# Optimization experiments

Hardware: AMD Instinct MI355X
Metric: run time of the kernel (lower is better)

## Reference

```python
import jax, jax.numpy as jnp
import numpy as np

P, B, L = 32, 64, 128
E, HB, HP = 64, 128, 128   # byte emb dim, byte GRU hidden, packet GRU hidden
PE = 2 * HB                # packet embedding dim = 256
LH = 128                   # attention linear hidden
NC = 10                    # num classes


def _gru_dir(x, w_ih, w_hh, b_ih, b_hh, reverse=False):
    # x: [T, N, E_in] -> outputs [T, N, H]; PyTorch GRU gate math, h0 = 0.
    H = w_hh.shape[1]
    xg = jnp.einsum('tne,ge->tng', x, w_ih) + b_ih  # precompute input gates [T,N,3H]
    if reverse:
        xg = xg[::-1]

    def step(h, xgt):
        hg = h @ w_hh.T + b_hh
        xr, xz, xn = jnp.split(xgt, 3, axis=-1)
        hr, hz, hn = jnp.split(hg, 3, axis=-1)
        r = jax.nn.sigmoid(xr + hr)
        z = jax.nn.sigmoid(xz + hz)
        n = jnp.tanh(xn + r * hn)
        h = (1.0 - z) * n + z * h
        return h, h

    h0 = jnp.zeros((x.shape[1], H), x.dtype)
    _, ys = jax.lax.scan(step, h0, xg)
    if reverse:
        ys = ys[::-1]
    return ys


def _bigru(x, wif, whf, bif, bhf, wib, whb, bib, bhb):
    f = _gru_dir(x, wif, whf, bif, bhf, reverse=False)
    b = _gru_dir(x, wib, whb, bib, bhb, reverse=True)
    return jnp.concatenate([f, b], axis=-1)


def setup_inputs() -> dict:
    key = jax.random.key(0)
    ks = jax.random.split(key, 32)
    rn = lambda k, shp: (jax.random.normal(k, shp, dtype=jnp.float32) * 0.05)
    inp = {}
    inp['flow'] = jax.random.randint(ks[0], (P, B, L), 0, 256, dtype=jnp.int64)
    inp['emb'] = rn(ks[1], (256, E))
    # byte biGRU (forward / backward dirs)
    inp['byte_wih_f'] = rn(ks[2], (3 * HB, E)); inp['byte_whh_f'] = rn(ks[3], (3 * HB, HB))
    inp['byte_bih_f'] = rn(ks[4], (3 * HB,));   inp['byte_bhh_f'] = rn(ks[5], (3 * HB,))
    inp['byte_wih_b'] = rn(ks[6], (3 * HB, E)); inp['byte_whh_b'] = rn(ks[7], (3 * HB, HB))
    inp['byte_bih_b'] = rn(ks[8], (3 * HB,));   inp['byte_bhh_b'] = rn(ks[9], (3 * HB,))
    # packet biGRU
    inp['pkt_wih_f'] = rn(ks[10], (3 * HP, PE)); inp['pkt_whh_f'] = rn(ks[11], (3 * HP, HP))
    inp['pkt_bih_f'] = rn(ks[12], (3 * HP,));    inp['pkt_bhh_f'] = rn(ks[13], (3 * HP,))
    inp['pkt_wih_b'] = rn(ks[14], (3 * HP, PE)); inp['pkt_whh_b'] = rn(ks[15], (3 * HP, HP))
    inp['pkt_bih_b'] = rn(ks[16], (3 * HP,));    inp['pkt_bhh_b'] = rn(ks[17], (3 * HP,))
    # byte attention (Linear(2HB->LH), Linear(LH->1))
    inp['ba_w1'] = rn(ks[18], (LH, 2 * HB)); inp['ba_b1'] = rn(ks[19], (LH,))
    inp['ba_w2'] = rn(ks[20], (1, LH));      inp['ba_b2'] = rn(ks[21], (1,))
    # packet attention (Linear(2HP->LH), Linear(LH->1))
    inp['pa_w1'] = rn(ks[22], (LH, 2 * HP)); inp['pa_b1'] = rn(ks[23], (LH,))
    inp['pa_w2'] = rn(ks[24], (1, LH));      inp['pa_b2'] = rn(ks[25], (1,))
    # final classifier
    inp['wf'] = rn(ks[26], (NC, 2 * HP)); inp['bf'] = rn(ks[27], (NC,))
    return inp


def reference(flow, emb,
              byte_wih_f, byte_whh_f, byte_bih_f, byte_bhh_f,
              byte_wih_b, byte_whh_b, byte_bih_b, byte_bhh_b,
              pkt_wih_f, pkt_whh_f, pkt_bih_f, pkt_bhh_f,
              pkt_wih_b, pkt_whh_b, pkt_bih_b, pkt_bhh_b,
              ba_w1, ba_b1, ba_w2, ba_b2,
              pa_w1, pa_b1, pa_w2, pa_b2,
              wf, bf):
    p, b, l = flow.shape
    x = emb[flow]                                   # [P,B,L,E]
    # batch the per-packet byte GRU across packets: [L, P*B, E]
    xb = x.transpose(2, 0, 1, 3).reshape(l, p * b, E)
    out = _bigru(xb, byte_wih_f, byte_whh_f, byte_bih_f, byte_bhh_f,
                 byte_wih_b, byte_whh_b, byte_bih_b, byte_bhh_b)  # [L, P*B, 2HB]
    out = out.reshape(l, p, b, 2 * HB)
    # Attention: tanh(lin1) -> lin2 -> softmax over dim=1 of the [L,B,1] view,
    # i.e. over the batch axis (faithful to the original code).
    h = jnp.tanh(jnp.einsum('lpbd,hd->lpbh', out, ba_w1) + ba_b1)
    score = jnp.einsum('lpbh,oh->lpbo', h, ba_w2) + ba_b2          # [L,P,B,1]
    attn = jax.nn.softmax(score, axis=2)
    packet_emb = (out * attn).sum(axis=0)                          # [P,B,2HB]
    # packet biGRU over packet sequence
    out2 = _bigru(packet_emb, pkt_wih_f, pkt_whh_f, pkt_bih_f, pkt_bhh_f,
                  pkt_wih_b, pkt_whh_b, pkt_bih_b, pkt_bhh_b)      # [P,B,2HP]
    h2 = jnp.tanh(jnp.einsum('pbd,hd->pbh', out2, pa_w1) + pa_b1)
    score2 = jnp.einsum('pbh,oh->pbo', h2, pa_w2) + pa_b2          # [P,B,1]
    attn2 = jax.nn.softmax(score2, axis=1)
    flow_emb = (out2 * attn2).sum(axis=1)                          # [P,2HP] (faithful sum over dim=1)
    return flow_emb @ wf.T + bf                                    # [P,NC]
```

## Files before the change

kernel.cpp:

```cpp
#include <hip/hip_runtime.h>
#include <hip/hip_bf16.h>
#include <hip/hip_fp16.h>
#include <cstdint>
#include <cstddef>


#define DINLINE __device__ __forceinline__

typedef _Float16 f16;
typedef f16 f16x8 __attribute__((ext_vector_type(8)));
typedef float f32x4 __attribute__((ext_vector_type(4)));

#define SCL_RZ (-1.44269504089f)
#define SCL_N (2.88539008178f)

static DINLINE float fast_tanh(float x) {
    const float e = __builtin_amdgcn_exp2f(2.88539008178f * x);
    return 1.0f - 2.0f * __builtin_amdgcn_rcpf(1.0f + e);
}

static DINLINE void lds_barrier() {
    asm volatile("s_waitcnt lgkmcnt(0)\n\ts_barrier" ::: "memory");
    __builtin_amdgcn_sched_barrier(0);
}

__global__ void k_tables_w1(const float* __restrict__ emb,
                            const float* __restrict__ wihF, const float* __restrict__ bihF,
                            const float* __restrict__ bhhF,
                            const float* __restrict__ wihB, const float* __restrict__ bihB,
                            const float* __restrict__ bhhB,
                            float4* __restrict__ tab4F, float4* __restrict__ tab4B,
                            const float* __restrict__ w1, f16* __restrict__ w1h) {
    if (blockIdx.x >= 512) {
        const int col = blockIdx.x - 512;
        const int k = threadIdx.x;
        if (k < 256)
            w1h[col * 256 + (k ^ ((col & 7) << 3))] =
                (f16)(SCL_N * w1[col * 256 + k]);
        return;
    }
    const int v = blockIdx.x & 255;
    const int dir = blockIdx.x >> 8;
    const float* wih = dir ? wihB : wihF;
    const float* bih = dir ? bihB : bihF;
    const float* bhh = dir ? bhhB : bhhF;
    float4* tab4 = dir ? tab4B : tab4F;
    __shared__ float er[64];
    __shared__ float sh[384];
    if (threadIdx.x < 64) er[threadIdx.x] = emb[v * 64 + threadIdx.x];
    __syncthreads();
    const int g = threadIdx.x;
    float acc = bih[g] + (g < 256 ? bhh[g] : 0.0f);
    #pragma unroll
    for (int e = 0; e < 64; ++e) acc = fmaf(wih[g * 64 + e], er[e], acc);
    sh[g] = acc * (g < 256 ? SCL_RZ : SCL_N);
    __syncthreads();
    if (g < 128) {
        float4 pk;
        pk.x = sh[g];
        pk.y = sh[g + 128];
        pk.z = sh[g + 256];
        pk.w = 0.f;
        tab4[v * 128 + g] = pk;
    }
}

struct TransArgs {
    const float* src[2];
    float* dst[2];
    int R[2];
    int C[2];
};
__global__ void k_transpose(TransArgs a) {
    const int m = blockIdx.y;
    const float* __restrict__ s = a.src[m];
    float* __restrict__ d = a.dst[m];
    const int R = a.R[m], C = a.C[m];
    const int total = R * C;
    for (int idx = blockIdx.x * blockDim.x + threadIdx.x; idx < total;
         idx += gridDim.x * blockDim.x) {
        const int r = idx / C, c = idx - r * C;
        d[c * R + r] = s[idx];
    }
}

__global__ __launch_bounds__(512, 1) void k_byte_gru(
    const int* __restrict__ flow,
    const float4* __restrict__ tab4F, const float4* __restrict__ tab4B,
    const float* __restrict__ whhF, const float* __restrict__ whhB,
    const float* __restrict__ bhhF, const float* __restrict__ bhhB,
    __half* __restrict__ hF, __half* __restrict__ hB) {
    const int dir = blockIdx.x & 1;
    const int chunk = blockIdx.x >> 1;
    const int row0 = chunk * 16;
    const int tid = threadIdx.x;
    const int wid = tid >> 6;
    const int lane = tid & 63;
    const int c = lane & 15;
    const int q = lane >> 4;
    const int j = wid * 16 + c;

    const float4* __restrict__ t4 = dir ? tab4B : tab4F;
    const float* __restrict__ whh = dir ? whhB : whhF;
    const float* __restrict__ bhh = dir ? bhhB : bhhF;
    __half* __restrict__ hout = dir ? hB : hF;

    __shared__ f16 hbuf[2][16 * 128];
    __shared__ int flow_lds[16][128];

    for (int i = tid; i < 16 * 128; i += 512)
        flow_lds[i >> 7][i & 127] = flow[row0 * 128 + i] & 255;
    for (int i = tid; i < 16 * 128; i += 512) hbuf[0][i] = (f16)0.f;

    f16x8 Bf[3][4];
    #pragma unroll
    for (int g = 0; g < 3; ++g) {
        const float scl = (g == 2) ? SCL_N : SCL_RZ;
        #pragma unroll
        for (int ks = 0; ks < 4; ++ks) {
            const float* src = whh + (size_t)(g * 128 + j) * 128 + ks * 32 + q * 8;
            f16x8 b;
            #pragma unroll
            for (int e = 0; e < 8; ++e) b[e] = (f16)(scl * src[e]);
            Bf[g][ks] = b;
        }
    }
    const float bh2 = SCL_N * bhh[j + 256];
    float hold[4];
    #pragma unroll
    for (int rr = 0; rr < 4; ++rr) hold[rr] = 0.f;
    __syncthreads();

    for (int t = 0; t < 128; ++t) {
        const int curb = t & 1, nxtb = curb ^ 1;
        const int tt = dir ? (127 - t) : t;

        float4 x4[4];
        #pragma unroll
        for (int rr = 0; rr < 4; ++rr)
            x4[rr] = t4[flow_lds[q * 4 + rr][tt] * 128 + j];

        f16x8 Af[4];
        #pragma unroll
        for (int ks = 0; ks < 4; ++ks) {
            const int kb = ks * 32 + q * 8;
            const int idx = c * 128 + (kb ^ ((c & 7) << 3));
            Af[ks] = *reinterpret_cast<const f16x8*>(&hbuf[curb][idx]);
        }

        f32x4 a0 = {0.f, 0.f, 0.f, 0.f};
        f32x4 a1 = {0.f, 0.f, 0.f, 0.f};
        f32x4 a2 = {0.f, 0.f, 0.f, 0.f};
        #pragma unroll
        for (int ks = 0; ks < 4; ++ks) {
            a0 = __builtin_amdgcn_mfma_f32_16x16x32_f16(Af[ks], Bf[0][ks], a0, 0, 0, 0);
            a1 = __builtin_amdgcn_mfma_f32_16x16x32_f16(Af[ks], Bf[1][ks], a1, 0, 0, 0);
            a2 = __builtin_amdgcn_mfma_f32_16x16x32_f16(Af[ks], Bf[2][ks], a2, 0, 0, 0);
        }

        #pragma unroll
        for (int rr = 0; rr < 4; ++rr) {
            const float e0 = __builtin_amdgcn_exp2f(x4[rr].x + a0[rr]);
            const float rg = __builtin_amdgcn_rcpf(1.0f + e0);
            const float e1 = __builtin_amdgcn_exp2f(x4[rr].y + a1[rr]);
            const float zg = __builtin_amdgcn_rcpf(1.0f + e1);
            const float e2 =
                __builtin_amdgcn_exp2f(x4[rr].z + rg * (a2[rr] + bh2));
            const float ng = fmaf(-2.0f, __builtin_amdgcn_rcpf(1.0f + e2), 1.0f);
            const float hn = fmaf(zg, hold[rr] - ng, ng);
            hold[rr] = hn;
            const int row = q * 4 + rr;
            hbuf[nxtb][row * 128 + (j ^ ((row & 7) << 3))] = (f16)hn;
        }
        lds_barrier();

        {
            const int row = tid >> 5;
            const int ho = (tid & 31) * 4;
            const int idx = row * 128 + (ho ^ ((row & 7) << 3));
            const uint2 v = *reinterpret_cast<const uint2*>(&hbuf[nxtb][idx]);
            *reinterpret_cast<uint2*>(
                &hout[((size_t)tt * 2048 + row0 + row) * 128 + ho]) = v;
        }
    }
}

__global__ __launch_bounds__(256, 1) void k_scores_attn(
    const __half* __restrict__ hF, const __half* __restrict__ hB,
    const f16* __restrict__ w1h,
    const float* __restrict__ b1, const float* __restrict__ w2,
    const float* __restrict__ b2, float* __restrict__ attn) {
    __shared__ f16 w1lds[128 * 256];
    __shared__ float sc[128];
    const int tid = threadIdx.x;
    {
        const uint2* src = reinterpret_cast<const uint2*>(w1h);
        uint2* dst = reinterpret_cast<uint2*>(w1lds);
        for (int i = tid; i < 8192; i += 256) dst[i] = src[i];
    }
    const int lane = tid & 63, w = tid >> 6;
    const int c = lane & 15, q = lane >> 4;

    float b1v[8], w2v[8];
    #pragma unroll
    for (int ct = 0; ct < 8; ++ct) {
        b1v[ct] = SCL_N * b1[ct * 16 + c];
        w2v[ct] = w2[ct * 16 + c];
    }
    const float b2v = b2[0];
    __syncthreads();

    for (int it = 0; it < 4; ++it) {
        const int pos0 = blockIdx.x * 512 + it * 128;

        f16x8 Af[2][8];
        #pragma unroll
        for (int pt = 0; pt < 2; ++pt) {
            const size_t pos = (size_t)pos0 + (w * 2 + pt) * 16 + c;
            const f16* hFp = (const f16*)(hF + pos * 128);
            const f16* hBp = (const f16*)(hB + pos * 128);
            #pragma unroll
            for (int ks = 0; ks < 4; ++ks)
                Af[pt][ks] = *reinterpret_cast<const f16x8*>(hFp + ks * 32 + q * 8);
            #pragma unroll
            for (int ks = 0; ks < 4; ++ks)
                Af[pt][4 + ks] = *reinterpret_cast<const f16x8*>(hBp + ks * 32 + q * 8);
        }

        float s[2][4] = {{0.f, 0.f, 0.f, 0.f}, {0.f, 0.f, 0.f, 0.f}};
        #pragma unroll
        for (int ct = 0; ct < 8; ++ct) {
            const int jj = ct * 16 + c;
            f16x8 Bfr[8];
            #pragma unroll
            for (int ks = 0; ks < 8; ++ks) {
                const int k = ks * 32 + q * 8;
                Bfr[ks] = *reinterpret_cast<const f16x8*>(
                    &w1lds[jj * 256 + (k ^ ((jj & 7) << 3))]);
            }
            #pragma unroll
            for (int pt = 0; pt < 2; ++pt) {
                f32x4 acc = {0.f, 0.f, 0.f, 0.f};
                #pragma unroll
                for (int ks = 0; ks < 8; ++ks)
                    acc = __builtin_amdgcn_mfma_f32_16x16x32_f16(Af[pt][ks],
                                                                 Bfr[ks], acc,
                                                                 0, 0, 0);
                #pragma unroll
                for (int rr = 0; rr < 4; ++rr) {
                    const float e2 = __builtin_amdgcn_exp2f(acc[rr] + b1v[ct]);
                    const float th =
                        fmaf(-2.0f, __builtin_amdgcn_rcpf(1.0f + e2), 1.0f);
                    s[pt][rr] = fmaf(w2v[ct], th, s[pt][rr]);
                }
            }
        }
        #pragma unroll
        for (int pt = 0; pt < 2; ++pt) {
            #pragma unroll
            for (int rr = 0; rr < 4; ++rr) {
                float v = s[pt][rr];
                v += __shfl_xor(v, 1);
                v += __shfl_xor(v, 2);
                v += __shfl_xor(v, 4);
                v += __shfl_xor(v, 8);
                if (c == 0) sc[(w * 2 + pt) * 16 + q * 4 + rr] = v + b2v;
            }
        }
        __syncthreads();
        if (tid < 128) {
            const float sv = sc[tid];
            float m = sv;
            for (int off = 32; off; off >>= 1) m = fmaxf(m, __shfl_xor(m, off));
            const float e = __expf(sv - m);
            float sum = e;
            for (int off = 32; off; off >>= 1) sum += __shfl_xor(sum, off);
            attn[pos0 + tid] = e / sum;
        }
        __syncthreads();
    }
}

__global__ __launch_bounds__(256) void k_packet_emb(
    const __half* __restrict__ hF, const __half* __restrict__ hB,
    const float* __restrict__ attn, float* __restrict__ pe) {
    const int tid = threadIdx.x;
    const int g = tid >> 6;
    const int lane = tid & 63;
    const int n = blockIdx.x * 4 + g;
    const bool isF = lane < 32;
    const int chunk = lane & 31;
    const __half* __restrict__ hsrc = (isF ? hF : hB) + (size_t)n * 128 + chunk * 4;
    float acc0 = 0.f, acc1 = 0.f, acc2 = 0.f, acc3 = 0.f;
    #pragma unroll 4
    for (int l = 0; l < 128; ++l) {
        const float wv = attn[l * 2048 + n];
        const uint2 u = *reinterpret_cast<const uint2*>(hsrc + (size_t)l * 2048 * 128);
        const f16* hv = reinterpret_cast<const f16*>(&u);
        acc0 = fmaf(wv, (float)hv[0], acc0);
        acc1 = fmaf(wv, (float)hv[1], acc1);
        acc2 = fmaf(wv, (float)hv[2], acc2);
        acc3 = fmaf(wv, (float)hv[3], acc3);
    }
    float4 o = {acc0, acc1, acc2, acc3};
    *reinterpret_cast<float4*>(&pe[n * 256 + (isF ? 0 : 128) + chunk * 4]) = o;
}

__global__ __launch_bounds__(384) void k_pkt_xg(
    const float* __restrict__ pe, const float* __restrict__ wihTF,
    const float* __restrict__ bihF, const float* __restrict__ bhhF,
    const float* __restrict__ wihTB, const float* __restrict__ bihB,
    const float* __restrict__ bhhB, float4* __restrict__ xg4F,
    float4* __restrict__ xg4B) {
    const int dir = blockIdx.y;
    const float* __restrict__ wihT = dir ? wihTB : wihTF;
    const float* __restrict__ bih = dir ? bihB : bihF;
    const float* __restrict__ bhh = dir ? bhhB : bhhF;
    float4* __restrict__ xg4 = dir ? xg4B : xg4F;
    const int rbase = blockIdx.x * 8;
    __shared__ float xrow[8][256];
    __shared__ float sh[8][384];
    for (int i = threadIdx.x; i < 8 * 256; i += 384)
        xrow[i >> 8][i & 255] = pe[rbase * 256 + i];
    __syncthreads();
    const int g = threadIdx.x;
    float acc[8];
    const float bias = bih[g] + (g < 256 ? bhh[g] : 0.0f);
    #pragma unroll
    for (int r = 0; r < 8; ++r) acc[r] = bias;
    for (int d = 0; d < 256; ++d) {
        const float w = wihT[d * 384 + g];
        #pragma unroll
        for (int r = 0; r < 8; ++r) acc[r] = fmaf(w, xrow[r][d], acc[r]);
    }
    const float scl = (g < 256) ? SCL_RZ : SCL_N;
    #pragma unroll
    for (int r = 0; r < 8; ++r) sh[r][g] = scl * acc[r];
    __syncthreads();
    for (int i = threadIdx.x; i < 8 * 128; i += 384) {
        const int r = i >> 7, jj = i & 127;
        float4 pk;
        pk.x = sh[r][jj];
        pk.y = sh[r][jj + 128];
        pk.z = sh[r][jj + 256];
        pk.w = 0.f;
        xg4[(size_t)(rbase + r) * 128 + jj] = pk;
    }
}

__global__ __launch_bounds__(512, 1) void k_pkt_gru(
    const float4* __restrict__ xg4F, const float4* __restrict__ xg4B,
    const float* __restrict__ whhF, const float* __restrict__ whhB,
    const float* __restrict__ bhhF, const float* __restrict__ bhhB,
    float* __restrict__ h2F, float* __restrict__ h2B) {
    const int dir = blockIdx.x & 1;
    const int chunk = blockIdx.x >> 1;
    const int row0 = chunk * 16;
    const int tid = threadIdx.x;
    const int wid = tid >> 6;
    const int lane = tid & 63;
    const int c = lane & 15;
    const int q = lane >> 4;
    const int j = wid * 16 + c;

    const float4* __restrict__ xg4 = dir ? xg4B : xg4F;
    const float* __restrict__ whh = dir ? whhB : whhF;
    const float* __restrict__ bhh = dir ? bhhB : bhhF;
    float* __restrict__ hout = dir ? h2B : h2F;

    __shared__ f16 hbuf[2][16 * 128];

    for (int i = tid; i < 16 * 128; i += 512) hbuf[0][i] = (f16)0.f;

    f16x8 Bf[3][4];
    #pragma unroll
    for (int g = 0; g < 3; ++g) {
        const float scl = (g == 2) ? SCL_N : SCL_RZ;
        #pragma unroll
        for (int ks = 0; ks < 4; ++ks) {
            const float* src = whh + (size_t)(g * 128 + j) * 128 + ks * 32 + q * 8;
            f16x8 b;
            #pragma unroll
            for (int e = 0; e < 8; ++e) b[e] = (f16)(scl * src[e]);
            Bf[g][ks] = b;
        }
    }
    const float bh2 = SCL_N * bhh[j + 256];
    float hold[4];
    #pragma unroll
    for (int rr = 0; rr < 4; ++rr) hold[rr] = 0.f;
    __syncthreads();

    for (int t = 0; t < 32; ++t) {
        const int curb = t & 1, nxtb = curb ^ 1;
        const int tt = dir ? (31 - t) : t;

        float4 x4[4];
        #pragma unroll
        for (int rr = 0; rr < 4; ++rr)
            x4[rr] = xg4[(size_t)(tt * 64 + row0 + q * 4 + rr) * 128 + j];

        f16x8 Af[4];
        #pragma unroll
        for (int ks = 0; ks < 4; ++ks) {
            const int kb = ks * 32 + q * 8;
            const int idx = c * 128 + (kb ^ ((c & 7) << 3));
            Af[ks] = *reinterpret_cast<const f16x8*>(&hbuf[curb][idx]);
        }

        f32x4 a0 = {0.f, 0.f, 0.f, 0.f};
        f32x4 a1 = {0.f, 0.f, 0.f, 0.f};
        f32x4 a2 = {0.f, 0.f, 0.f, 0.f};
        #pragma unroll
        for (int ks = 0; ks < 4; ++ks) {
            a0 = __builtin_amdgcn_mfma_f32_16x16x32_f16(Af[ks], Bf[0][ks], a0, 0, 0, 0);
            a1 = __builtin_amdgcn_mfma_f32_16x16x32_f16(Af[ks], Bf[1][ks], a1, 0, 0, 0);
            a2 = __builtin_amdgcn_mfma_f32_16x16x32_f16(Af[ks], Bf[2][ks], a2, 0, 0, 0);
        }

        #pragma unroll
        for (int rr = 0; rr < 4; ++rr) {
            const float e0 = __builtin_amdgcn_exp2f(x4[rr].x + a0[rr]);
            const float rg = __builtin_amdgcn_rcpf(1.0f + e0);
            const float e1 = __builtin_amdgcn_exp2f(x4[rr].y + a1[rr]);
            const float zg = __builtin_amdgcn_rcpf(1.0f + e1);
            const float e2 =
                __builtin_amdgcn_exp2f(x4[rr].z + rg * (a2[rr] + bh2));
            const float ng = fmaf(-2.0f, __builtin_amdgcn_rcpf(1.0f + e2), 1.0f);
            const float hn = fmaf(zg, hold[rr] - ng, ng);
            hold[rr] = hn;
            const int row = q * 4 + rr;
            hbuf[nxtb][row * 128 + (j ^ ((row & 7) << 3))] = (f16)hn;
            hout[((size_t)tt * 64 + row0 + row) * 128 + j] = hn;
        }
        lds_barrier();
    }
}

__global__ __launch_bounds__(128) void k_scores2(
    const float* __restrict__ h2F, const float* __restrict__ h2B,
    const float* __restrict__ paw1,
    const float* __restrict__ pab1, const float* __restrict__ paw2,
    const float* __restrict__ pab2, float* __restrict__ scores2) {
    const int n = blockIdx.x;
    const int tid = threadIdx.x;
    __shared__ float x[256];
    __shared__ float red[2];
    x[tid] = h2F[n * 128 + tid];
    x[tid + 128] = h2B[n * 128 + tid];
    __syncthreads();
    float acc = pab1[tid];
    const float* wr = paw1 + tid * 256;
    #pragma unroll 8
    for (int d = 0; d < 256; ++d) acc = fmaf(wr[d], x[d], acc);
    float s = paw2[tid] * fast_tanh(acc);
    s += __shfl_xor(s, 1);
    s += __shfl_xor(s, 2);
    s += __shfl_xor(s, 4);
    s += __shfl_xor(s, 8);
    s += __shfl_xor(s, 16);
    s += __shfl_xor(s, 32);
    if ((tid & 63) == 0) red[tid >> 6] = s;
    __syncthreads();
    if (tid == 0) scores2[n] = red[0] + red[1] + pab2[0];
}

__global__ __launch_bounds__(256) void k_final3(
    const float* __restrict__ h2F, const float* __restrict__ h2B,
    const float* __restrict__ scores2, const float* __restrict__ wf,
    const float* __restrict__ bfv, float* __restrict__ outp) {
    const int p = blockIdx.x;
    const int tid = threadIdx.x;
    __shared__ float sc[64];
    __shared__ float femb[256];
    __shared__ float red[64];

    if (tid < 64) {
        const float s = scores2[p * 64 + tid];
        float m = s;
        for (int off = 32; off; off >>= 1) m = fmaxf(m, __shfl_xor(m, off));
        const float e = __expf(s - m);
        float sum = e;
        for (int off = 32; off; off >>= 1) sum += __shfl_xor(sum, off);
        sc[tid] = e / sum;
    }
    __syncthreads();

    {
        const float* __restrict__ hsrc = (tid < 128) ? h2F : h2B;
        const int d = tid & 127;
        float acc = 0.f;
        for (int b = 0; b < 64; ++b)
            acc = fmaf(sc[b], hsrc[(p * 64 + b) * 128 + d], acc);
        femb[tid] = acc;
    }
    __syncthreads();

    const float fv = femb[tid];
    #pragma unroll
    for (int c = 0; c < 10; ++c) {
        float s = fv * wf[c * 256 + tid];
        s += __shfl_xor(s, 1);
        s += __shfl_xor(s, 2);
        s += __shfl_xor(s, 4);
        s += __shfl_xor(s, 8);
        s += __shfl_xor(s, 16);
        s += __shfl_xor(s, 32);
        if ((tid & 63) == 0) red[(c << 2) | (tid >> 6)] = s;
        __syncthreads();
        if (tid == 0)
            outp[p * 10 + c] = bfv[c] + red[c << 2] + red[(c << 2) | 1] +
                               red[(c << 2) | 2] + red[(c << 2) | 3];
        __syncthreads();
    }
}

extern "C" void kernel_launch(void* const* d_in, const int* in_sizes, int n_in,
                              void* d_out, int out_size, void* d_ws,
                              size_t ws_size, hipStream_t stream) {
    const int* flow = (const int*)d_in[0];
    const float* emb = (const float*)d_in[1];
    const float* byte_wih_f = (const float*)d_in[2];
    const float* byte_whh_f = (const float*)d_in[3];
    const float* byte_bih_f = (const float*)d_in[4];
    const float* byte_bhh_f = (const float*)d_in[5];
    const float* byte_wih_b = (const float*)d_in[6];
    const float* byte_whh_b = (const float*)d_in[7];
    const float* byte_bih_b = (const float*)d_in[8];
    const float* byte_bhh_b = (const float*)d_in[9];
    const float* pkt_wih_f = (const float*)d_in[10];
    const float* pkt_whh_f = (const float*)d_in[11];
    const float* pkt_bih_f = (const float*)d_in[12];
    const float* pkt_bhh_f = (const float*)d_in[13];
    const float* pkt_wih_b = (const float*)d_in[14];
    const float* pkt_whh_b = (const float*)d_in[15];
    const float* pkt_bih_b = (const float*)d_in[16];
    const float* pkt_bhh_b = (const float*)d_in[17];
    const float* ba_w1 = (const float*)d_in[18];
    const float* ba_b1 = (const float*)d_in[19];
    const float* ba_w2 = (const float*)d_in[20];
    const float* ba_b2 = (const float*)d_in[21];
    const float* pa_w1 = (const float*)d_in[22];
    const float* pa_b1 = (const float*)d_in[23];
    const float* pa_w2 = (const float*)d_in[24];
    const float* pa_b2 = (const float*)d_in[25];
    const float* wf = (const float*)d_in[26];
    const float* bf = (const float*)d_in[27];

    char* base = (char*)d_ws;
    size_t off = 0;
    auto allocf = [&](size_t nf) -> float* {
        float* p = (float*)(base + off);
        off += nf * sizeof(float);
        return p;
    };
    auto alloch = [&](size_t nh) -> __half* {
        off = (off + 255) & ~(size_t)255;
        __half* p = (__half*)(base + off);
        off += nh * sizeof(__half);
        return p;
    };
    float* wihTpF = allocf(256 * 384);
    float* wihTpB = allocf(256 * 384);
    float* attn = allocf(262144);
    float* pe = allocf(2048 * 256);
    float4* tab4F = (float4*)allocf(256 * 128 * 4);
    float4* tab4B = (float4*)allocf(256 * 128 * 4);
    float4* xg4F = (float4*)allocf((size_t)2048 * 128 * 4);
    float4* xg4B = (float4*)allocf((size_t)2048 * 128 * 4);
    float* h2F = allocf(32 * 64 * 128);
    float* h2B = allocf(32 * 64 * 128);
    float* scores2 = allocf(2048);
    __half* w1h = alloch(128 * 256);
    __half* hF = alloch((size_t)128 * 2048 * 128);
    __half* hB = alloch((size_t)128 * 2048 * 128);
    if (off > ws_size) return;
    (void)in_sizes; (void)n_in; (void)out_size;

    k_tables_w1<<<640, 384, 0, stream>>>(emb, byte_wih_f, byte_bih_f,
                                         byte_bhh_f, byte_wih_b, byte_bih_b,
                                         byte_bhh_b, tab4F, tab4B, ba_w1,
                                         (f16*)w1h);

    TransArgs ta;
    ta.src[0] = pkt_wih_f; ta.dst[0] = wihTpF; ta.R[0] = 384; ta.C[0] = 256;
    ta.src[1] = pkt_wih_b; ta.dst[1] = wihTpB; ta.R[1] = 384; ta.C[1] = 256;
    k_transpose<<<dim3(96, 2), 256, 0, stream>>>(ta);

    k_byte_gru<<<256, 512, 0, stream>>>(flow, tab4F, tab4B, byte_whh_f,
                                        byte_whh_b, byte_bhh_f, byte_bhh_b, hF,
                                        hB);

    k_scores_attn<<<512, 256, 0, stream>>>(hF, hB, (const f16*)w1h, ba_b1,
                                           ba_w2, ba_b2, attn);
    k_packet_emb<<<512, 256, 0, stream>>>(hF, hB, attn, pe);

    k_pkt_xg<<<dim3(256, 2), 384, 0, stream>>>(pe, wihTpF, pkt_bih_f,
                                               pkt_bhh_f, wihTpB, pkt_bih_b,
                                               pkt_bhh_b, xg4F, xg4B);
    k_pkt_gru<<<8, 512, 0, stream>>>(xg4F, xg4B, pkt_whh_f, pkt_whh_b,
                                     pkt_bhh_f, pkt_bhh_b, h2F, h2B);
    k_scores2<<<2048, 128, 0, stream>>>(h2F, h2B, pa_w1, pa_b1, pa_w2, pa_b2,
                                        scores2);
    k_final3<<<32, 256, 0, stream>>>(h2F, h2B, scores2, wf, bf, (float*)d_out);
}
```

Before: 287.7 us.

## Fuse transpose into table kernel, streamline byte GRU gathers and stores, retune attention grids

Folds the packet weight transpose into the table-building kernel, which removes one launch. In the byte GRU, flow indices are stored transposed and pre-shifted so one int4 LDS read gives four byte offsets, and each lane writes its hidden state straight to global memory instead of re-reading LDS after the barrier. The scores kernel handles half as many positions per block across twice as many blocks, and the packet-embedding loop batches eight loads before accumulating to expose more memory parallelism. The direct per-element half stores are narrower and less coalesced than the old 8-byte row stores, and doubling the scores blocks repeats the weight load into LDS more often.

```diff
diff --git a/kernel.cpp b/kernel.cpp
--- a/kernel.cpp
+++ b/kernel.cpp
@@ -30,7 +30,20 @@
                             const float* __restrict__ wihB, const float* __restrict__ bihB,
                             const float* __restrict__ bhhB,
                             float4* __restrict__ tab4F, float4* __restrict__ tab4B,
-                            const float* __restrict__ w1, f16* __restrict__ w1h) {
+                            const float* __restrict__ w1, f16* __restrict__ w1h,
+                            const float* __restrict__ pwihF, const float* __restrict__ pwihB,
+                            float* __restrict__ wihTpF, float* __restrict__ wihTpB) {
+    if (blockIdx.x >= 640) {
+        const int bid = blockIdx.x - 640;
+        const int m = bid / 96, bx = bid % 96;
+        const float* __restrict__ s = m ? pwihB : pwihF;
+        float* __restrict__ d = m ? wihTpB : wihTpF;
+        for (int idx = bx * 384 + threadIdx.x; idx < 384 * 256; idx += 96 * 384) {
+            const int r = idx >> 8, c = idx & 255;
+            d[c * 384 + r] = s[idx];
+        }
+        return;
+    }
     if (blockIdx.x >= 512) {
         const int col = blockIdx.x - 512;
         const int k = threadIdx.x;
@@ -62,25 +75,6 @@
         pk.z = sh[g + 256];
         pk.w = 0.f;
         tab4[v * 128 + g] = pk;
-    }
-}
-
-struct TransArgs {
-    const float* src[2];
-    float* dst[2];
-    int R[2];
-    int C[2];
-};
-__global__ void k_transpose(TransArgs a) {
-    const int m = blockIdx.y;
-    const float* __restrict__ s = a.src[m];
-    float* __restrict__ d = a.dst[m];
-    const int R = a.R[m], C = a.C[m];
-    const int total = R * C;
-    for (int idx = blockIdx.x * blockDim.x + threadIdx.x; idx < total;
-         idx += gridDim.x * blockDim.x) {
-        const int r = idx / C, c = idx - r * C;
-        d[c * R + r] = s[idx];
     }
 }
 
@@ -100,16 +94,19 @@
     const int q = lane >> 4;
     const int j = wid * 16 + c;
 
-    const float4* __restrict__ t4 = dir ? tab4B : tab4F;
+    const char* __restrict__ t4j =
+        reinterpret_cast<const char*>(dir ? tab4B : tab4F) + (j << 4);
     const float* __restrict__ whh = dir ? whhB : whhF;
     const float* __restrict__ bhh = dir ? bhhB : bhhF;
     __half* __restrict__ hout = dir ? hB : hF;
 
     __shared__ f16 hbuf[2][16 * 128];
-    __shared__ int flow_lds[16][128];
-
-    for (int i = tid; i < 16 * 128; i += 512)
-        flow_lds[i >> 7][i & 127] = flow[row0 * 128 + i] & 255;
+    __shared__ int flow_lds[128][16];
+
+    for (int i = tid; i < 16 * 128; i += 512) {
+        const int row = i >> 7, t = i & 127;
+        flow_lds[t][row] = (flow[row0 * 128 + i] & 255) << 11;
+    }
     for (int i = tid; i < 16 * 128; i += 512) hbuf[0][i] = (f16)0.f;
 
     f16x8 Bf[3][4];
@@ -135,10 +132,12 @@
         const int curb = t & 1, nxtb = curb ^ 1;
         const int tt = dir ? (127 - t) : t;
 
+        const int4 off4 = *reinterpret_cast<const int4*>(&flow_lds[tt][q * 4]);
         float4 x4[4];
-        #pragma unroll
-        for (int rr = 0; rr < 4; ++rr)
-            x4[rr] = t4[flow_lds[q * 4 + rr][tt] * 128 + j];
+        x4[0] = *reinterpret_cast<const float4*>(t4j + off4.x);
+        x4[1] = *reinterpret_cast<const float4*>(t4j + off4.y);
+        x4[2] = *reinterpret_cast<const float4*>(t4j + off4.z);
+        x4[3] = *reinterpret_cast<const float4*>(t4j + off4.w);
 
         f16x8 Af[4];
         #pragma unroll
@@ -158,6 +157,7 @@
             a2 = __builtin_amdgcn_mfma_f32_16x16x32_f16(Af[ks], Bf[2][ks], a2, 0, 0, 0);
         }
 
+        __half* hp = hout + ((size_t)tt * 2048 + row0 + q * 4) * 128 + j;
         #pragma unroll
         for (int rr = 0; rr < 4; ++rr) {
             const float e0 = __builtin_amdgcn_exp2f(x4[rr].x + a0[rr]);
@@ -171,17 +171,9 @@
             hold[rr] = hn;
             const int row = q * 4 + rr;
             hbuf[nxtb][row * 128 + (j ^ ((row & 7) << 3))] = (f16)hn;
+            hp[rr * 128] = (__half)hn;
         }
         lds_barrier();
-
-        {
-            const int row = tid >> 5;
-            const int ho = (tid & 31) * 4;
-            const int idx = row * 128 + (ho ^ ((row & 7) << 3));
-            const uint2 v = *reinterpret_cast<const uint2*>(&hbuf[nxtb][idx]);
-            *reinterpret_cast<uint2*>(
-                &hout[((size_t)tt * 2048 + row0 + row) * 128 + ho]) = v;
-        }
     }
 }
 
@@ -210,8 +202,8 @@
     const float b2v = b2[0];
     __syncthreads();
 
-    for (int it = 0; it < 4; ++it) {
-        const int pos0 = blockIdx.x * 512 + it * 128;
+    for (int it = 0; it < 2; ++it) {
+        const int pos0 = blockIdx.x * 256 + it * 128;
 
         f16x8 Af[2][8];
         #pragma unroll
@@ -292,15 +284,23 @@
     const int chunk = lane & 31;
     const __half* __restrict__ hsrc = (isF ? hF : hB) + (size_t)n * 128 + chunk * 4;
     float acc0 = 0.f, acc1 = 0.f, acc2 = 0.f, acc3 = 0.f;
-    #pragma unroll 4
-    for (int l = 0; l < 128; ++l) {
-        const float wv = attn[l * 2048 + n];
-        const uint2 u = *reinterpret_cast<const uint2*>(hsrc + (size_t)l * 2048 * 128);
-        const f16* hv = reinterpret_cast<const f16*>(&u);
-        acc0 = fmaf(wv, (float)hv[0], acc0);
-        acc1 = fmaf(wv, (float)hv[1], acc1);
-        acc2 = fmaf(wv, (float)hv[2], acc2);
-        acc3 = fmaf(wv, (float)hv[3], acc3);
+    for (int l0 = 0; l0 < 128; l0 += 8) {
+        float wv[8];
+        uint2 u[8];
+        #pragma unroll
+        for (int k = 0; k < 8; ++k) {
+            wv[k] = attn[(l0 + k) * 2048 + n];
+            u[k] = *reinterpret_cast<const uint2*>(hsrc +
+                                                   (size_t)(l0 + k) * 2048 * 128);
+        }
+        #pragma unroll
+        for (int k = 0; k < 8; ++k) {
+            const f16* hv = reinterpret_cast<const f16*>(&u[k]);
+            acc0 = fmaf(wv[k], (float)hv[0], acc0);
+            acc1 = fmaf(wv[k], (float)hv[1], acc1);
+            acc2 = fmaf(wv[k], (float)hv[2], acc2);
+            acc3 = fmaf(wv[k], (float)hv[3], acc3);
+        }
     }
     float4 o = {acc0, acc1, acc2, acc3};
     *reinterpret_cast<float4*>(&pe[n * 256 + (isF ? 0 : 128) + chunk * 4]) = o;
@@ -577,22 +577,18 @@
     if (off > ws_size) return;
     (void)in_sizes; (void)n_in; (void)out_size;
 
-    k_tables_w1<<<640, 384, 0, stream>>>(emb, byte_wih_f, byte_bih_f,
+    k_tables_w1<<<832, 384, 0, stream>>>(emb, byte_wih_f, byte_bih_f,
                                          byte_bhh_f, byte_wih_b, byte_bih_b,
                                          byte_bhh_b, tab4F, tab4B, ba_w1,
-                                         (f16*)w1h);
-
-    TransArgs ta;
-    ta.src[0] = pkt_wih_f; ta.dst[0] = wihTpF; ta.R[0] = 384; ta.C[0] = 256;
-    ta.src[1] = pkt_wih_b; ta.dst[1] = wihTpB; ta.R[1] = 384; ta.C[1] = 256;
-    k_transpose<<<dim3(96, 2), 256, 0, stream>>>(ta);
+                                         (f16*)w1h, pkt_wih_f, pkt_wih_b,
+                                         wihTpF, wihTpB);
 
     k_byte_gru<<<256, 512, 0, stream>>>(flow, tab4F, tab4B, byte_whh_f,
                                         byte_whh_b, byte_bhh_f, byte_bhh_b, hF,
                                         hB);
 
-    k_scores_attn<<<512, 256, 0, stream>>>(hF, hB, (const f16*)w1h, ba_b1,
-                                           ba_w2, ba_b2, attn);
+    k_scores_attn<<<1024, 256, 0, stream>>>(hF, hB, (const f16*)w1h, ba_b1,
+                                            ba_w2, ba_b2, attn);
     k_packet_emb<<<512, 256, 0, stream>>>(hF, hB, attn, pe);
 
     k_pkt_xg<<<dim3(256, 2), 384, 0, stream>>>(pe, wihTpF, pkt_bih_f,
```

Measured after the change: 282.5 us. Within noise of the previous version (-1.8%).
